# Optimization experiments

Measured on AMD Instinct MI355X. Metric: run time of the kernel, lower is better.

Reference implementation:

```python
import jax, jax.numpy as jnp
import numpy as np
import math

H = 16
D_MODEL = 1024
D_K = D_MODEL // H


def setup_inputs() -> dict:
    key = jax.random.key(0)
    ks = jax.random.split(key, 12)
    B, S, D = 2, 2048, D_MODEL
    s = 1.0 / math.sqrt(D)
    inp = {
        "query": jax.random.normal(ks[0], (B, S, D), jnp.float32),
        "key": jax.random.normal(ks[1], (B, S, D), jnp.float32),
        "value": jax.random.normal(ks[2], (B, S, D), jnp.float32),
        "mask": jnp.ones((B, 1, S), jnp.int32),
        "wq": jax.random.normal(ks[3], (D, D), jnp.float32) * s,
        "bq": jnp.zeros((D,), jnp.float32),
        "wk": jax.random.normal(ks[4], (D, D), jnp.float32) * s,
        "bk": jnp.zeros((D,), jnp.float32),
        "wv": jax.random.normal(ks[5], (D, D), jnp.float32) * s,
        "bv": jnp.zeros((D,), jnp.float32),
        "wo": jax.random.normal(ks[6], (D, D), jnp.float32) * s,
        "bo": jnp.zeros((D,), jnp.float32),
    }
    return inp


def _split_heads(x, B, S):
    # [B, S, D] -> [B, H, S, D_K]
    return x.reshape(B, S, H, D_K).transpose(0, 2, 1, 3)


def reference(query, key, value, mask, wq, bq, wk, bk, wv, bv, wo, bo):
    B, S, D = query.shape
    q = _split_heads(query @ wq.T + bq, B, S)
    k = _split_heads(key @ wk.T + bk, B, S)
    v = _split_heads(value @ wv.T + bv, B, S)
    # scores: [B, H, S, S]
    scores = jnp.einsum("bhqd,bhkd->bhqk", q, k) / math.sqrt(D_K)
    m = mask[:, None, :, :]  # [B,1,1,S] after unsqueeze(1)
    scores = jnp.where(m == 0, jnp.float32(-1e9), scores)
    p_attn = jax.nn.softmax(scores, axis=-1)  # dropout = identity (eval)
    x = jnp.einsum("bhqk,bhkd->bhqd", p_attn, v)
    x = x.transpose(0, 2, 1, 3).reshape(B, S, D)
    return x @ wo.T + bo
```

## Files before the change

### kernel.cpp

```cpp
#include <hip/hip_runtime.h>
#include <hip/hip_bf16.h>

#define DEV __device__ __forceinline__

typedef __attribute__((ext_vector_type(8))) short bf16x8;
typedef __attribute__((ext_vector_type(4))) float f32x4;
typedef __attribute__((ext_vector_type(4))) unsigned u32x4;
typedef unsigned short u16;
typedef __attribute__((ext_vector_type(8))) unsigned short u16x8;

DEV u16 f2bf(float f) {
  union { float f; unsigned u; } v; v.f = f;
  unsigned r = v.u + 0x7fffu + ((v.u >> 16) & 1u);
  return (u16)(r >> 16);
}
DEV unsigned cvtpk(float a, float b) {
  unsigned r;
  asm("v_cvt_pk_bf16_f32 %0, %1, %2" : "=v"(r) : "v"(a), "v"(b));
  return r;
}

DEV void gl_lds16(const void* g, void* l) {
  __builtin_amdgcn_global_load_lds(
      (const __attribute__((address_space(1))) void*)g,
      (__attribute__((address_space(3))) void*)l, 16, 0, 0);
}

#define MFMA16(a, b, c) __builtin_amdgcn_mfma_f32_16x16x32_bf16((a), (b), (c), 0, 0, 0)

#define QSCALE 0.18033688011112042f

__global__ __launch_bounds__(256) void conv_all(
    const float* __restrict__ q, const float* __restrict__ k, const float* __restrict__ v,
    const float* __restrict__ wq, const float* __restrict__ wk,
    const float* __restrict__ wv, const float* __restrict__ wo,
    u16* __restrict__ dst)
{
  const long i = (long)(blockIdx.x * 256 + threadIdx.x) * 8;
  const float* src; long off;
  if      (i < 4194304)  { src = q;  off = i; }
  else if (i < 8388608)  { src = k;  off = i - 4194304; }
  else if (i < 12582912) { src = v;  off = i - 8388608; }
  else if (i < 13631488) { src = wq; off = i - 12582912; }
  else if (i < 14680064) { src = wk; off = i - 13631488; }
  else if (i < 15728640) { src = wv; off = i - 14680064; }
  else                   { src = wo; off = i - 15728640; }
  float4 a = *(const float4*)(src + off);
  float4 b = *(const float4*)(src + off + 4);
  u16x8 r;
  r[0] = f2bf(a.x); r[1] = f2bf(a.y); r[2] = f2bf(a.z); r[3] = f2bf(a.w);
  r[4] = f2bf(b.x); r[5] = f2bf(b.y); r[6] = f2bf(b.z); r[7] = f2bf(b.w);
  *(u16x8*)(dst + i) = r;
}

DEV void gemm_core(const u16* __restrict__ A, const u16* __restrict__ W,
                   u16* As, u16* Bs, int row0, int col0, f32x4 acc[4][4])
{
  const int tid  = threadIdx.x;
  const int wave = tid >> 6, lane = tid & 63;
  const int wm = wave >> 1, wn = wave & 1;
  const int lr = lane & 15, lk = lane >> 4;
  #pragma unroll 1
  for (int kt = 0; kt < 32; ++kt) {
    const int k0 = kt * 32;
    __syncthreads();
    #pragma unroll
    for (int i = 0; i < 2; ++i) {
      const int blk = i * 4 + wave;
      const int c = blk * 64 + lane;
      const int r = c >> 2, kc = (c & 3) * 8;
      gl_lds16(A + (row0 + r) * 1024 + k0 + kc, As + blk * 512 + lane * 8);
      gl_lds16(W + (col0 + r) * 1024 + k0 + kc, Bs + blk * 512 + lane * 8);
    }
    __syncthreads();
    bf16x8 a[4], b[4];
    #pragma unroll
    for (int m = 0; m < 4; ++m)
      a[m] = *(const bf16x8*)(As + (wm * 64 + m * 16 + lr) * 32 + lk * 8);
    #pragma unroll
    for (int n = 0; n < 4; ++n)
      b[n] = *(const bf16x8*)(Bs + (wn * 64 + n * 16 + lr) * 32 + lk * 8);
    __builtin_amdgcn_s_setprio(1);
    #pragma unroll
    for (int m = 0; m < 4; ++m)
      #pragma unroll
      for (int n = 0; n < 4; ++n)
        acc[m][n] = MFMA16(a[m], b[n], acc[m][n]);
    __builtin_amdgcn_s_setprio(0);
  }
}

__global__ __launch_bounds__(256, 3) void gemm_qkv(
    const u16* __restrict__ xq, const u16* __restrict__ xk, const u16* __restrict__ xv,
    const u16* __restrict__ wqb, const u16* __restrict__ wkb, const u16* __restrict__ wvb,
    const float* __restrict__ bq, const float* __restrict__ bk, const float* __restrict__ bv,
    u16* __restrict__ Qo, u16* __restrict__ Ko, u16* __restrict__ Vt)
{
  __shared__ u16 As[4096], Bs[4096];
  const int z = blockIdx.z;
  const u16* A = (z == 0) ? xq : (z == 1) ? xk : xv;
  const u16* W = (z == 0) ? wqb : (z == 1) ? wkb : wvb;
  const float* bias = (z == 0) ? bq : (z == 1) ? bk : bv;
  const int row0 = blockIdx.x * 128, col0 = blockIdx.y * 128;
  f32x4 acc[4][4] = {};
  gemm_core(A, W, As, Bs, row0, col0, acc);
  const int tid = threadIdx.x, wave = tid >> 6, lane = tid & 63;
  const int wm = wave >> 1, wn = wave & 1, lr = lane & 15, lq = lane >> 4;
  if (z < 2) {
    const float sc = (z == 0) ? QSCALE : 1.0f;
    u16* outp = (z == 0) ? Qo : Ko;
    #pragma unroll
    for (int m = 0; m < 4; ++m)
      #pragma unroll
      for (int n = 0; n < 4; ++n) {
        const int cc = col0 + wn * 64 + n * 16 + lr;
        const float bb = bias[cc];
        #pragma unroll
        for (int j = 0; j < 4; ++j) {
          const int rr = row0 + wm * 64 + m * 16 + lq * 4 + j;
          outp[rr * 1024 + cc] = f2bf((acc[m][n][j] + bb) * sc);
        }
      }
  } else {
    #pragma unroll
    for (int m = 0; m < 4; ++m)
      #pragma unroll
      for (int n = 0; n < 4; ++n) {
        const int cc = col0 + wn * 64 + n * 16 + lr;
        const float bb = bias[cc];
        const int h = cc >> 6, dk = cc & 63;
        const int rr = row0 + wm * 64 + m * 16 + lq * 4;
        const int b_ = rr >> 11, s_ = rr & 2047;
        uint2 pr;
        pr.x = cvtpk(acc[m][n][0] + bb, acc[m][n][1] + bb);
        pr.y = cvtpk(acc[m][n][2] + bb, acc[m][n][3] + bb);
        *(uint2*)(Vt + (((long)(b_ * 16 + h) * 64 + dk) << 11) + s_) = pr;
      }
  }
}

__global__ __launch_bounds__(256, 4) void flash(
    const u16* __restrict__ Q, const u16* __restrict__ K,
    const u16* __restrict__ Vt, const int* __restrict__ mask,
    u16* __restrict__ X)
{
  __shared__ u16 Ks[2][4096], Vs[2][4096];
  const int qt = blockIdx.x, bh = blockIdx.y;
  const int b = bh >> 4, h = bh & 15;
  const int tid = threadIdx.x, wave = tid >> 6, lane = tid & 63;
  const int lr = lane & 15, lq = lane >> 4;
  const int qbase = qt * 64 + wave * 16;

  const u16* Kg = K + (long)b * 2048 * 1024 + h * 64;
  const u16* Vg = Vt + (long)(b * 16 + h) * 64 * 2048;
  const int* mb = mask + b * 2048;

  const u16* Qrow = Q + (long)(b * 2048 + qbase + lr) * 1024 + h * 64 + lq * 8;
  const bf16x8 bq0 = *(const bf16x8*)Qrow;
  const bf16x8 bq1 = *(const bf16x8*)(Qrow + 32);

  const int r1  = tid >> 3;
  const int c41 = (tid & 7) ^ (r1 & 7);
  const long gK1 = (long)r1 * 1024 + c41 * 8;
  const long gV1 = (long)r1 * 2048 + c41 * 8;
  const int xv    = lq ^ (lr & 7);
  const int offLo = (lr * 8 + xv) * 8;
  const int offHi = (lr * 8 + (xv ^ 4)) * 8;

  float lsum = 0.f;
  f32x4 o[4] = {};

  gl_lds16(Kg + gK1,             &Ks[0][tid * 8]);
  gl_lds16(Kg + gK1 + 32 * 1024, &Ks[0][tid * 8 + 2048]);
  gl_lds16(Vg + gV1,             &Vs[0][tid * 8]);
  gl_lds16(Vg + gV1 + 32 * 2048, &Vs[0][tid * 8 + 2048]);
  __syncthreads();

  #pragma unroll 1
  for (int t = 0; t < 32; ++t) {
    const int cur = t & 1, nxt = cur ^ 1;
    const int kv0 = t * 64;
    if (t < 31) {
      const long kq = kv0 + 64;
      gl_lds16(Kg + kq * 1024 + gK1,        &Ks[nxt][tid * 8]);
      gl_lds16(Kg + (kq + 32) * 1024 + gK1, &Ks[nxt][tid * 8 + 2048]);
      gl_lds16(Vg + kq + gV1,               &Vs[nxt][tid * 8]);
      gl_lds16(Vg + kq + gV1 + 32 * 2048,   &Vs[nxt][tid * 8 + 2048]);
    }
    const u16* kb = Ks[cur];
    f32x4 st[4];
    __builtin_amdgcn_s_setprio(1);
    #pragma unroll
    for (int n = 0; n < 4; ++n) {
      const bf16x8 klo = *(const bf16x8*)(kb + n * 1024 + offLo);
      const bf16x8 khi = *(const bf16x8*)(kb + n * 1024 + offHi);
      f32x4 z = {};
      z = MFMA16(klo, bq0, z);
      z = MFMA16(khi, bq1, z);
      st[n] = z;
    }
    __builtin_amdgcn_s_setprio(0);
    const int mv = mb[kv0 + lane];
    if (!__all(mv != 0)) {
      #pragma unroll
      for (int n = 0; n < 4; ++n) {
        const int4 mm = *(const int4*)(mb + kv0 + n * 16 + lq * 4);
        st[n][0] = mm.x ? st[n][0] : -1e9f;
        st[n][1] = mm.y ? st[n][1] : -1e9f;
        st[n][2] = mm.z ? st[n][2] : -1e9f;
        st[n][3] = mm.w ? st[n][3] : -1e9f;
      }
    }
    #pragma unroll
    for (int n = 0; n < 4; ++n)
      #pragma unroll
      for (int j = 0; j < 4; ++j) {
        st[n][j] = __builtin_amdgcn_exp2f(fminf(st[n][j], 30.0f));
        lsum += st[n][j];
      }
    unsigned pk0[2], pk1[2], pk2[2], pk3[2];
    pk0[0] = cvtpk(st[0][0], st[0][1]); pk0[1] = cvtpk(st[0][2], st[0][3]);
    pk1[0] = cvtpk(st[1][0], st[1][1]); pk1[1] = cvtpk(st[1][2], st[1][3]);
    pk2[0] = cvtpk(st[2][0], st[2][1]); pk2[1] = cvtpk(st[2][2], st[2][3]);
    pk3[0] = cvtpk(st[3][0], st[3][1]); pk3[1] = cvtpk(st[3][2], st[3][3]);
    const int sl0 = lr + 32 * (lq & 1);
    const int sl1 = sl0 + 16;
    const bool hiN = (lq >> 1) != 0;
    u32x4 w0, w1;
    {
      const unsigned a0 = __shfl(pk0[0], sl0, 64), b0 = __shfl(pk1[0], sl0, 64);
      const unsigned a1 = __shfl(pk0[1], sl0, 64), b1 = __shfl(pk1[1], sl0, 64);
      const unsigned a2 = __shfl(pk0[0], sl1, 64), b2 = __shfl(pk1[0], sl1, 64);
      const unsigned a3 = __shfl(pk0[1], sl1, 64), b3 = __shfl(pk1[1], sl1, 64);
      w0[0] = hiN ? b0 : a0; w0[1] = hiN ? b1 : a1;
      w0[2] = hiN ? b2 : a2; w0[3] = hiN ? b3 : a3;
    }
    {
      const unsigned a0 = __shfl(pk2[0], sl0, 64), b0 = __shfl(pk3[0], sl0, 64);
      const unsigned a1 = __shfl(pk2[1], sl0, 64), b1 = __shfl(pk3[1], sl0, 64);
      const unsigned a2 = __shfl(pk2[0], sl1, 64), b2 = __shfl(pk3[0], sl1, 64);
      const unsigned a3 = __shfl(pk2[1], sl1, 64), b3 = __shfl(pk3[1], sl1, 64);
      w1[0] = hiN ? b0 : a0; w1[1] = hiN ? b1 : a1;
      w1[2] = hiN ? b2 : a2; w1[3] = hiN ? b3 : a3;
    }
    union { u32x4 u; bf16x8 h; } cb0, cb1;
    cb0.u = w0; cb1.u = w1;
    const u16* vb = Vs[cur];
    __builtin_amdgcn_s_setprio(1);
    #pragma unroll
    for (int n = 0; n < 4; ++n) {
      const bf16x8 vlo = *(const bf16x8*)(vb + n * 1024 + offLo);
      const bf16x8 vhi = *(const bf16x8*)(vb + n * 1024 + offHi);
      o[n] = MFMA16(vlo, cb0.h, o[n]);
      o[n] = MFMA16(vhi, cb1.h, o[n]);
    }
    __builtin_amdgcn_s_setprio(0);
    __syncthreads();
  }

  lsum += __shfl_xor(lsum, 16, 64);
  lsum += __shfl_xor(lsum, 32, 64);
  const float inv = 1.0f / lsum;
  const long xrow = (long)(b * 2048 + qbase + lr) * 1024 + h * 64;
  #pragma unroll
  for (int n = 0; n < 4; ++n) {
    *(unsigned*)(X + xrow + n * 16 + lq * 4)     = cvtpk(o[n][0] * inv, o[n][1] * inv);
    *(unsigned*)(X + xrow + n * 16 + lq * 4 + 2) = cvtpk(o[n][2] * inv, o[n][3] * inv);
  }
}

__global__ __launch_bounds__(256, 3) void gemm_out(
    const u16* __restrict__ X, const u16* __restrict__ Wo,
    const float* __restrict__ bo, float* __restrict__ out)
{
  __shared__ u16 As[2048], Bs[4096];
  const int row0 = blockIdx.x * 64, col0 = blockIdx.y * 128;
  const int tid = threadIdx.x, wave = tid >> 6, lane = tid & 63;
  const int lr = lane & 15, lk = lane >> 4, lq = lane >> 4;
  f32x4 acc[4][2] = {};
  #pragma unroll 1
  for (int kt = 0; kt < 32; ++kt) {
    const int k0 = kt * 32;
    __syncthreads();
    {
      const int r = tid >> 2, kc = (tid & 3) * 8;
      gl_lds16(X + (row0 + r) * 1024 + k0 + kc, As + tid * 8);
    }
    #pragma unroll
    for (int i = 0; i < 2; ++i) {
      const int c = i * 256 + tid;
      const int r = c >> 2, kc = (c & 3) * 8;
      gl_lds16(Wo + (col0 + r) * 1024 + k0 + kc, Bs + c * 8);
    }
    __syncthreads();
    bf16x8 a[4], b[2];
    #pragma unroll
    for (int m = 0; m < 4; ++m)
      a[m] = *(const bf16x8*)(As + (m * 16 + lr) * 32 + lk * 8);
    #pragma unroll
    for (int n = 0; n < 2; ++n)
      b[n] = *(const bf16x8*)(Bs + (wave * 32 + n * 16 + lr) * 32 + lk * 8);
    __builtin_amdgcn_s_setprio(1);
    #pragma unroll
    for (int m = 0; m < 4; ++m)
      #pragma unroll
      for (int n = 0; n < 2; ++n)
        acc[m][n] = MFMA16(a[m], b[n], acc[m][n]);
    __builtin_amdgcn_s_setprio(0);
  }
  #pragma unroll
  for (int m = 0; m < 4; ++m)
    #pragma unroll
    for (int n = 0; n < 2; ++n) {
      const int cc = col0 + wave * 32 + n * 16 + lr;
      const float bb = bo[cc];
      #pragma unroll
      for (int j = 0; j < 4; ++j) {
        const int rr = row0 + m * 16 + lq * 4 + j;
        out[rr * 1024 + cc] = acc[m][n][j] + bb;
      }
    }
}

extern "C" void kernel_launch(void* const* d_in, const int* in_sizes, int n_in,
                              void* d_out, int out_size, void* d_ws, size_t ws_size,
                              hipStream_t stream) {
  const float* q   = (const float*)d_in[0];
  const float* k   = (const float*)d_in[1];
  const float* v   = (const float*)d_in[2];
  const int*   msk = (const int*)d_in[3];
  const float* wq  = (const float*)d_in[4];
  const float* bq  = (const float*)d_in[5];
  const float* wk  = (const float*)d_in[6];
  const float* bk  = (const float*)d_in[7];
  const float* wv  = (const float*)d_in[8];
  const float* bv  = (const float*)d_in[9];
  const float* wo  = (const float*)d_in[10];
  const float* bo  = (const float*)d_in[11];

  u16* ws  = (u16*)d_ws;
  u16* xq  = ws;
  u16* xk  = ws + 4194304;
  u16* xv  = ws + 8388608;
  u16* wqb = ws + 12582912;
  u16* wkb = ws + 13631488;
  u16* wvb = ws + 14680064;
  u16* wob = ws + 15728640;
  u16* Qb  = ws + 16777216;
  u16* Kb  = ws + 20971520;
  u16* Vtb = ws + 25165824;
  u16* Xb  = ws + 29360128;

  conv_all<<<8192, 256, 0, stream>>>(q, k, v, wq, wk, wv, wo, ws);
  gemm_qkv<<<dim3(32, 8, 3), 256, 0, stream>>>(xq, xk, xv, wqb, wkb, wvb,
                                               bq, bk, bv, Qb, Kb, Vtb);
  flash<<<dim3(32, 32), 256, 0, stream>>>(Qb, Kb, Vtb, msk, Xb);
  gemm_out<<<dim3(64, 8), 256, 0, stream>>>(Xb, wob, bo, (float*)d_out);
}
```

Baseline: 241.8 us.

## Switch flash attention to 32x32x16 MFMA with two-wave blocks and permlane swaps

Rewrites the flash attention inner loop to use 32x32x16 bf16 MFMA tiles. Each wave now handles 32 query rows, and each block has 2 waves (128 threads) instead of 4, so the 64-row query tile per block is unchanged. The P matrix is rearranged into the B-operand layout with v_permlane32_swap instead of the many __shfl calls plus selects. The aim is fewer MFMA instructions and cheaper cross-lane data movement, at the cost of fewer waves per block and more register pressure for the 16-wide accumulators.

```diff
diff --git a/kernel.cpp b/kernel.cpp
--- a/kernel.cpp
+++ b/kernel.cpp
@@ -5,6 +5,7 @@
 
 typedef __attribute__((ext_vector_type(8))) short bf16x8;
 typedef __attribute__((ext_vector_type(4))) float f32x4;
+typedef __attribute__((ext_vector_type(16))) float f32x16;
 typedef __attribute__((ext_vector_type(4))) unsigned u32x4;
 typedef unsigned short u16;
 typedef __attribute__((ext_vector_type(8))) unsigned short u16x8;
@@ -27,6 +28,7 @@
 }
 
 #define MFMA16(a, b, c) __builtin_amdgcn_mfma_f32_16x16x32_bf16((a), (b), (c), 0, 0, 0)
+#define MFMA32(a, b, c) __builtin_amdgcn_mfma_f32_32x32x16_bf16((a), (b), (c), 0, 0, 0)
 
 #define QSCALE 0.18033688011112042f
 
@@ -139,41 +141,45 @@
   }
 }
 
-__global__ __launch_bounds__(256, 4) void flash(
+__global__ __launch_bounds__(128, 2) void flash(
     const u16* __restrict__ Q, const u16* __restrict__ K,
     const u16* __restrict__ Vt, const int* __restrict__ mask,
     u16* __restrict__ X)
 {
   __shared__ u16 Ks[2][4096], Vs[2][4096];
   const int qt = blockIdx.x, bh = blockIdx.y;
-  const int b = bh >> 4, h = bh & 15;
+  const int b = bh >> 4, hd = bh & 15;
   const int tid = threadIdx.x, wave = tid >> 6, lane = tid & 63;
-  const int lr = lane & 15, lq = lane >> 4;
-  const int qbase = qt * 64 + wave * 16;
-
-  const u16* Kg = K + (long)b * 2048 * 1024 + h * 64;
-  const u16* Vg = Vt + (long)(b * 16 + h) * 64 * 2048;
+  const int col = lane & 31, half = lane >> 5;
+  const int qbase = qt * 64 + wave * 32;
+
+  const u16* Kg = K + (long)b * 2048 * 1024 + hd * 64;
+  const u16* Vg = Vt + (long)(b * 16 + hd) * 64 * 2048;
   const int* mb = mask + b * 2048;
 
-  const u16* Qrow = Q + (long)(b * 2048 + qbase + lr) * 1024 + h * 64 + lq * 8;
-  const bf16x8 bq0 = *(const bf16x8*)Qrow;
-  const bf16x8 bq1 = *(const bf16x8*)(Qrow + 32);
-
-  const int r1  = tid >> 3;
-  const int c41 = (tid & 7) ^ (r1 & 7);
-  const long gK1 = (long)r1 * 1024 + c41 * 8;
-  const long gV1 = (long)r1 * 2048 + c41 * 8;
-  const int xv    = lq ^ (lr & 7);
-  const int offLo = (lr * 8 + xv) * 8;
-  const int offHi = (lr * 8 + (xv ^ 4)) * 8;
+  const u16* Qrow = Q + (long)(b * 2048 + qbase + col) * 1024 + hd * 64 + half * 8;
+  bf16x8 bq[4];
+  #pragma unroll
+  for (int s = 0; s < 4; ++s) bq[s] = *(const bf16x8*)(Qrow + s * 16);
+
+  int gK[4], gV[4], ld[4];
+  #pragma unroll
+  for (int p = 0; p < 4; ++p) {
+    const int c = p * 128 + tid, row = c >> 3, ch = (c & 7) ^ (row & 7);
+    gK[p] = row * 1024 + ch * 8;
+    gV[p] = row * 2048 + ch * 8;
+    ld[p] = c * 8;
+  }
+  const int cx = col & 7;
 
   float lsum = 0.f;
-  f32x4 o[4] = {};
-
-  gl_lds16(Kg + gK1,             &Ks[0][tid * 8]);
-  gl_lds16(Kg + gK1 + 32 * 1024, &Ks[0][tid * 8 + 2048]);
-  gl_lds16(Vg + gV1,             &Vs[0][tid * 8]);
-  gl_lds16(Vg + gV1 + 32 * 2048, &Vs[0][tid * 8 + 2048]);
+  f32x16 o0 = {}, o1 = {};
+
+  #pragma unroll
+  for (int p = 0; p < 4; ++p) {
+    gl_lds16(Kg + gK[p], &Ks[0][ld[p]]);
+    gl_lds16(Vg + gV[p], &Vs[0][ld[p]]);
+  }
   __syncthreads();
 
   #pragma unroll 1
@@ -181,91 +187,90 @@
     const int cur = t & 1, nxt = cur ^ 1;
     const int kv0 = t * 64;
     if (t < 31) {
-      const long kq = kv0 + 64;
-      gl_lds16(Kg + kq * 1024 + gK1,        &Ks[nxt][tid * 8]);
-      gl_lds16(Kg + (kq + 32) * 1024 + gK1, &Ks[nxt][tid * 8 + 2048]);
-      gl_lds16(Vg + kq + gV1,               &Vs[nxt][tid * 8]);
-      gl_lds16(Vg + kq + gV1 + 32 * 2048,   &Vs[nxt][tid * 8 + 2048]);
+      const u16* Kn = Kg + (long)(kv0 + 64) * 1024;
+      const u16* Vn = Vg + kv0 + 64;
+      #pragma unroll
+      for (int p = 0; p < 4; ++p) {
+        gl_lds16(Kn + gK[p], &Ks[nxt][ld[p]]);
+        gl_lds16(Vn + gV[p], &Vs[nxt][ld[p]]);
+      }
     }
     const u16* kb = Ks[cur];
-    f32x4 st[4];
+    f32x16 sv[2];
     __builtin_amdgcn_s_setprio(1);
     #pragma unroll
-    for (int n = 0; n < 4; ++n) {
-      const bf16x8 klo = *(const bf16x8*)(kb + n * 1024 + offLo);
-      const bf16x8 khi = *(const bf16x8*)(kb + n * 1024 + offHi);
-      f32x4 z = {};
-      z = MFMA16(klo, bq0, z);
-      z = MFMA16(khi, bq1, z);
-      st[n] = z;
+    for (int v = 0; v < 2; ++v) {
+      f32x16 z = {};
+      #pragma unroll
+      for (int s = 0; s < 4; ++s) {
+        const int off = ((v * 32 + col) * 8 + ((s * 2 + half) ^ cx)) * 8;
+        z = MFMA32(*(const bf16x8*)(kb + off), bq[s], z);
+      }
+      sv[v] = z;
     }
     __builtin_amdgcn_s_setprio(0);
     const int mv = mb[kv0 + lane];
     if (!__all(mv != 0)) {
       #pragma unroll
-      for (int n = 0; n < 4; ++n) {
-        const int4 mm = *(const int4*)(mb + kv0 + n * 16 + lq * 4);
-        st[n][0] = mm.x ? st[n][0] : -1e9f;
-        st[n][1] = mm.y ? st[n][1] : -1e9f;
-        st[n][2] = mm.z ? st[n][2] : -1e9f;
-        st[n][3] = mm.w ? st[n][3] : -1e9f;
-      }
-    }
-    #pragma unroll
-    for (int n = 0; n < 4; ++n)
-      #pragma unroll
-      for (int j = 0; j < 4; ++j) {
-        st[n][j] = __builtin_amdgcn_exp2f(fminf(st[n][j], 30.0f));
-        lsum += st[n][j];
-      }
-    unsigned pk0[2], pk1[2], pk2[2], pk3[2];
-    pk0[0] = cvtpk(st[0][0], st[0][1]); pk0[1] = cvtpk(st[0][2], st[0][3]);
-    pk1[0] = cvtpk(st[1][0], st[1][1]); pk1[1] = cvtpk(st[1][2], st[1][3]);
-    pk2[0] = cvtpk(st[2][0], st[2][1]); pk2[1] = cvtpk(st[2][2], st[2][3]);
-    pk3[0] = cvtpk(st[3][0], st[3][1]); pk3[1] = cvtpk(st[3][2], st[3][3]);
-    const int sl0 = lr + 32 * (lq & 1);
-    const int sl1 = sl0 + 16;
-    const bool hiN = (lq >> 1) != 0;
-    u32x4 w0, w1;
-    {
-      const unsigned a0 = __shfl(pk0[0], sl0, 64), b0 = __shfl(pk1[0], sl0, 64);
-      const unsigned a1 = __shfl(pk0[1], sl0, 64), b1 = __shfl(pk1[1], sl0, 64);
-      const unsigned a2 = __shfl(pk0[0], sl1, 64), b2 = __shfl(pk1[0], sl1, 64);
-      const unsigned a3 = __shfl(pk0[1], sl1, 64), b3 = __shfl(pk1[1], sl1, 64);
-      w0[0] = hiN ? b0 : a0; w0[1] = hiN ? b1 : a1;
-      w0[2] = hiN ? b2 : a2; w0[3] = hiN ? b3 : a3;
-    }
-    {
-      const unsigned a0 = __shfl(pk2[0], sl0, 64), b0 = __shfl(pk3[0], sl0, 64);
-      const unsigned a1 = __shfl(pk2[1], sl0, 64), b1 = __shfl(pk3[1], sl0, 64);
-      const unsigned a2 = __shfl(pk2[0], sl1, 64), b2 = __shfl(pk3[0], sl1, 64);
-      const unsigned a3 = __shfl(pk2[1], sl1, 64), b3 = __shfl(pk3[1], sl1, 64);
-      w1[0] = hiN ? b0 : a0; w1[1] = hiN ? b1 : a1;
-      w1[2] = hiN ? b2 : a2; w1[3] = hiN ? b3 : a3;
-    }
-    union { u32x4 u; bf16x8 h; } cb0, cb1;
-    cb0.u = w0; cb1.u = w1;
+      for (int v = 0; v < 2; ++v)
+        #pragma unroll
+        for (int gq = 0; gq < 4; ++gq) {
+          const int4 mm = *(const int4*)(mb + kv0 + v * 32 + gq * 8 + half * 4);
+          sv[v][gq * 4 + 0] = mm.x ? sv[v][gq * 4 + 0] : -1e9f;
+          sv[v][gq * 4 + 1] = mm.y ? sv[v][gq * 4 + 1] : -1e9f;
+          sv[v][gq * 4 + 2] = mm.z ? sv[v][gq * 4 + 2] : -1e9f;
+          sv[v][gq * 4 + 3] = mm.w ? sv[v][gq * 4 + 3] : -1e9f;
+        }
+    }
+    #pragma unroll
+    for (int v = 0; v < 2; ++v)
+      #pragma unroll
+      for (int g = 0; g < 16; ++g) {
+        sv[v][g] = __builtin_amdgcn_exp2f(fminf(sv[v][g], 30.0f));
+        lsum += sv[v][g];
+      }
+    unsigned q16[2][8];
+    #pragma unroll
+    for (int v = 0; v < 2; ++v)
+      #pragma unroll
+      for (int p = 0; p < 8; ++p)
+        q16[v][p] = cvtpk(sv[v][2 * p], sv[v][2 * p + 1]);
+    union { u32x4 u; bf16x8 h; } pb[4];
+    #pragma unroll
+    for (int tt = 0; tt < 4; ++tt) {
+      const int v = tt >> 1, base = (tt & 1) * 4;
+      unsigned A0 = q16[v][base + 0], A1 = q16[v][base + 1];
+      unsigned A2 = q16[v][base + 2], A3 = q16[v][base + 3];
+      asm("v_permlane32_swap_b32 %0, %1" : "+v"(A0), "+v"(A2));
+      asm("v_permlane32_swap_b32 %0, %1" : "+v"(A1), "+v"(A3));
+      pb[tt].u[0] = A0; pb[tt].u[1] = A1; pb[tt].u[2] = A2; pb[tt].u[3] = A3;
+    }
     const u16* vb = Vs[cur];
     __builtin_amdgcn_s_setprio(1);
     #pragma unroll
-    for (int n = 0; n < 4; ++n) {
-      const bf16x8 vlo = *(const bf16x8*)(vb + n * 1024 + offLo);
-      const bf16x8 vhi = *(const bf16x8*)(vb + n * 1024 + offHi);
-      o[n] = MFMA16(vlo, cb0.h, o[n]);
-      o[n] = MFMA16(vhi, cb1.h, o[n]);
+    for (int tt = 0; tt < 4; ++tt) {
+      const int off0 = ((0 * 32 + col) * 8 + ((tt * 2 + half) ^ cx)) * 8;
+      const int off1 = ((1 * 32 + col) * 8 + ((tt * 2 + half) ^ cx)) * 8;
+      o0 = MFMA32(*(const bf16x8*)(vb + off0), pb[tt].h, o0);
+      o1 = MFMA32(*(const bf16x8*)(vb + off1), pb[tt].h, o1);
     }
     __builtin_amdgcn_s_setprio(0);
     __syncthreads();
   }
 
-  lsum += __shfl_xor(lsum, 16, 64);
   lsum += __shfl_xor(lsum, 32, 64);
   const float inv = 1.0f / lsum;
-  const long xrow = (long)(b * 2048 + qbase + lr) * 1024 + h * 64;
-  #pragma unroll
-  for (int n = 0; n < 4; ++n) {
-    *(unsigned*)(X + xrow + n * 16 + lq * 4)     = cvtpk(o[n][0] * inv, o[n][1] * inv);
-    *(unsigned*)(X + xrow + n * 16 + lq * 4 + 2) = cvtpk(o[n][2] * inv, o[n][3] * inv);
+  const long xrow = (long)(b * 2048 + qbase + col) * 1024 + hd * 64;
+  #pragma unroll
+  for (int gq = 0; gq < 4; ++gq) {
+    const int g = gq * 4;
+    uint2 p0, p1;
+    p0.x = cvtpk(o0[g] * inv, o0[g + 1] * inv);
+    p0.y = cvtpk(o0[g + 2] * inv, o0[g + 3] * inv);
+    *(uint2*)(X + xrow + gq * 8 + half * 4) = p0;
+    p1.x = cvtpk(o1[g] * inv, o1[g + 1] * inv);
+    p1.y = cvtpk(o1[g + 2] * inv, o1[g + 3] * inv);
+    *(uint2*)(X + xrow + 32 + gq * 8 + half * 4) = p1;
   }
 }
 
@@ -354,6 +359,6 @@
   conv_all<<<8192, 256, 0, stream>>>(q, k, v, wq, wk, wv, wo, ws);
   gemm_qkv<<<dim3(32, 8, 3), 256, 0, stream>>>(xq, xk, xv, wqb, wkb, wvb,
                                                bq, bk, bv, Qb, Kb, Vtb);
-  flash<<<dim3(32, 32), 256, 0, stream>>>(Qb, Kb, Vtb, msk, Xb);
+  flash<<<dim3(32, 32), 128, 0, stream>>>(Qb, Kb, Vtb, msk, Xb);
   gemm_out<<<dim3(64, 8), 256, 0, stream>>>(Xb, wob, bo, (float*)d_out);
 }
```

After: 245.7 us. Within noise of the previous version (+1.6%).
